# Optimization experiments

Measured on AMD Instinct MI355X. Metric: run time of the kernel, lower is better.

## Reference

```python
import jax, jax.numpy as jnp
import numpy as np
import math

EPS = 1e-9
NORM = 1.0 / math.sqrt(20.0)  # num_neighbours=20 default


def _mixing(x1, x2, B, W, b):
    # nn.Bilinear (no bias): x_bi[n,k] = sum_ij x1[n,i] B[k,i,j] x2[n,j]
    x_bi = jnp.einsum('ni,kij->nkj', x1, B)
    x_bi = jnp.einsum('nkj,nj->nk', x_bi, x2)
    x = jnp.concatenate([x1, x2, x_bi], axis=-1)
    return x @ W.T + b


def _rowstd(x):
    # torch.std default: unbiased (ddof=1)
    return jnp.std(x, axis=1, ddof=1, keepdims=True)


def setup_inputs() -> dict:
    key = jax.random.key(0)
    N, E = 100000, 2000000
    DN, DE, DA_N, DA_E = 32, 32, 3, 1
    ks = jax.random.split(key, 24)

    def nrm(k, shape, fan_in):
        return jax.random.normal(k, shape, dtype=jnp.float32) / np.sqrt(fan_in)

    inp = {
        'xn': jax.random.normal(ks[0], (N, DN), dtype=jnp.float32),
        'xn_attr': jax.random.normal(ks[1], (N, DA_N), dtype=jnp.float32),
        'xe_attr': jax.random.normal(ks[2], (E, DA_E), dtype=jnp.float32),
        'xe_src': jax.random.randint(ks[3], (E,), 0, N),
        'xe_dst': jax.random.randint(ks[4], (E,), 0, N),
        # fc1: Linear(1, xe_dim); fc2: Linear(1, xn_dim)
        'W_fc1': nrm(ks[5], (DE, 1), 1), 'b_fc1': jnp.zeros((DE,), jnp.float32),
        'W_fc2': nrm(ks[6], (DN, 1), 1), 'b_fc2': jnp.zeros((DN,), jnp.float32),
        # mix_xn: Mixing(DN, DA_N, DN)
        'B_mix_xn': nrm(ks[7], (DN, DN, DA_N), DN * DA_N),
        'W_mix_xn': nrm(ks[8], (DN, 2 * DN + DA_N), 2 * DN + DA_N),
        'b_mix_xn': jnp.zeros((DN,), jnp.float32),
        # nodes_to_edges.mix: Mixing(DN, DN, DN)
        'B_n2e': nrm(ks[9], (DN, DN, DN), DN * DN),
        'W_n2e': nrm(ks[10], (DN, 3 * DN), 3 * DN),
        'b_n2e': jnp.zeros((DN,), jnp.float32),
        # mix_xe: Mixing(DE, DA_E, DE)
        'B_mix_xe': nrm(ks[11], (DE, DE, DA_E), DE * DA_E),
        'W_mix_xe': nrm(ks[12], (DE, 2 * DE + DA_E), 2 * DE + DA_E),
        'b_mix_xe': jnp.zeros((DE,), jnp.float32),
        # edges_to_nodes.mix: Mixing(DE, DE, DE)
        'B_e2n': nrm(ks[13], (DE, DE, DE), DE * DE),
        'W_e2n': nrm(ks[14], (DE, 3 * DE), 3 * DE),
        'b_e2n': jnp.zeros((DE,), jnp.float32),
    }
    return inp


def reference(xn, xn_attr, xe_attr, xe_src, xe_dst,
              W_fc1, b_fc1, W_fc2, b_fc2,
              B_mix_xn, W_mix_xn, b_mix_xn,
              B_n2e, W_n2e, b_n2e,
              B_mix_xe, W_mix_xe, b_mix_xe,
              B_e2n, W_e2n, b_e2n):
    n_nodes = xn.shape[0]
    # node mixing + per-row std norm
    xn = _mixing(xn, xn_attr, B_mix_xn, W_mix_xn, b_mix_xn)
    xn = xn / (_rowstd(xn) + EPS)
    # fc1 weight: [E, xe_dim]
    w1 = jax.nn.silu(xe_attr @ W_fc1.T + b_fc1)
    # NodesToEdges: gather -> grad/ave -> mixing
    xg, xd = xn[xe_src], xn[xe_dst]
    xe = _mixing(w1 * (xg - xd), w1 * (xg + xd) * 0.5, B_n2e, W_n2e, b_n2e)
    xe = _mixing(xe, xe_attr, B_mix_xe, W_mix_xe, b_mix_xe)
    xe = xe / (_rowstd(xe) + EPS)
    # fc2 weight: [E, xn_dim]
    w2 = jax.nn.silu(xe_attr @ W_fc2.T + b_fc2)
    # EdgesToNodes: scatter-add over dst/src, diff/sum, mixing
    wxe = w2 * xe
    xn1 = jax.ops.segment_sum(wxe, xe_dst, num_segments=n_nodes) * NORM
    xn2 = jax.ops.segment_sum(wxe, xe_src, num_segments=n_nodes) * NORM
    xn = _mixing(xn1 - xn2, xn1 + xn2, B_e2n, W_e2n, b_e2n)
    xn = jax.nn.silu(xn)
    xn = xn / (_rowstd(xn) + EPS)
    return xn
```

## Files before the change

### kernel.cpp

```cpp
#include <hip/hip_runtime.h>
#include <hip/hip_bf16.h>

#define N_NODES 100000
#define N_EDGES 2000000
#define EPS 1e-9f
#define NORMC 0.22360679774997896f

#define BKSZ   256
#define NBK1   391
#define NBK    782
#define NSB    256
#define CE     7813
#define NITEMS 4000000

typedef short s8 __attribute__((ext_vector_type(8)));
typedef float f4 __attribute__((ext_vector_type(4)));

__device__ __forceinline__ float silu_f(float x) {
    return x / (1.0f + __expf(-x));
}

__device__ __forceinline__ ushort f2bfu(float f) {
    union { __hip_bfloat16 b; ushort u; } cv;
    cv.b = __float2bfloat16(f);
    return cv.u;
}

__device__ __forceinline__ uint pkbf(float lo, float hi) {
    float2 t; t.x = lo; t.y = hi;
    union { __hip_bfloat162 b; uint u; } cv;
    cv.b = __float22bfloat162_rn(t);
    return cv.u;
}


__device__ float mext(const float* __restrict__ W, const float* __restrict__ B,
                      const float* __restrict__ bias, int n, int i, int j) {
    if (i < 32 && j < 32) {
        float r = 0.f;
        #pragma unroll
        for (int m = 0; m < 32; ++m) r += W[n*96 + 64 + m] * B[m*1024 + i*32 + j];
        return r;
    }
    if (i < 32) return W[n*96 + i];
    if (j < 32) return W[n*96 + 32 + j];
    return bias[n];
}

__global__ void prep_kernel(const float* __restrict__ W_n2e, const float* __restrict__ B_n2e,
                            const float* __restrict__ b_n2e,
                            const float* __restrict__ W_e2n, const float* __restrict__ B_e2n,
                            const float* __restrict__ b_e2n,
                            const float* __restrict__ W_mix_xn, const float* __restrict__ B_mix_xn,
                            const float* __restrict__ b_mix_xn,
                            const float* __restrict__ W_mix_xe, const float* __restrict__ B_mix_xe,
                            const float* __restrict__ b_mix_xe,
                            ushort* __restrict__ MF, ushort* __restrict__ MG,
                            float* __restrict__ BpN, float* __restrict__ WxE,
                            float* __restrict__ CtE) {
    int t = blockIdx.x * blockDim.x + threadIdx.x;
    if (t < 69632) {
        int u = (t < 34816) ? t : t - 34816;
        int tt = u & 7, lane = (u >> 3) & 63, rest = u >> 9;
        int nt = rest & 1, kk = rest >> 1;
        int n = nt*16 + (lane & 15);
        int kl = ((lane >> 4) & 3) * 8 + tt;
        int i, j;
        if (kk < 33) { i = kk; j = kl; } else { i = kl; j = 32; }
        if (t < 34816) MF[u] = f2bfu(mext(W_n2e, B_n2e, b_n2e, n, i, j));
        else           MG[u] = f2bfu(mext(W_e2n, B_e2n, b_e2n, n, i, j));
    } else if (t < 73856) {
        int u = t - 69632;
        int k = u & 31, ij = u >> 5;
        int i = ij >> 2, j = ij & 3;
        float r;
        if (i < 32 && j < 3) {
            r = 0.f;
            #pragma unroll
            for (int m = 0; m < 32; ++m) r += W_mix_xn[k*67 + 35 + m] * B_mix_xn[m*96 + i*3 + j];
        } else if (i < 32 && j == 3) {
            r = W_mix_xn[k*67 + i];
        } else if (i == 32 && j < 3) {
            r = W_mix_xn[k*67 + 32 + j];
        } else {
            r = b_mix_xn[k];
        }
        BpN[ij*32 + k] = r;
    } else if (t < 74912) {
        int u = t - 73856;
        int k = u & 31, i = u >> 5;
        WxE[i*32 + k] = (i < 32) ? W_mix_xe[k*65 + i] : b_mix_xe[k];
    } else if (t < 75968) {
        int u = t - 74912;
        int k = u & 31, i = u >> 5;
        float r;
        if (i < 32) {
            r = 0.f;
            #pragma unroll
            for (int m = 0; m < 32; ++m) r += W_mix_xe[k*65 + 33 + m] * B_mix_xe[m*32 + i];
        } else {
            r = W_mix_xe[k*65 + 32];
        }
        CtE[i*32 + k] = r;
    }
}

__global__ void zero_kernel(float4* __restrict__ p, int n4) {
    int i = blockIdx.x * blockDim.x + threadIdx.x;
    int stride = gridDim.x * blockDim.x;
    float4 z = {0.f, 0.f, 0.f, 0.f};
    for (; i < n4; i += stride) p[i] = z;
}

__global__ __launch_bounds__(256) void node_kernel(
    const float* __restrict__ xn, const float* __restrict__ xn_attr,
    const float* __restrict__ BpN, float* __restrict__ xn_norm) {
    int n = blockIdx.x * 256 + threadIdx.x;
    if (n >= N_NODES) return;
    float x[33];
    const float4* xr = (const float4*)(xn + (size_t)n * 32);
    #pragma unroll
    for (int q = 0; q < 8; ++q) {
        float4 v = xr[q];
        x[q*4+0] = v.x; x[q*4+1] = v.y; x[q*4+2] = v.z; x[q*4+3] = v.w;
    }
    x[32] = 1.f;
    float at[4];
    at[0] = xn_attr[n*3]; at[1] = xn_attr[n*3+1]; at[2] = xn_attr[n*3+2]; at[3] = 1.f;

    float acc[32];
    #pragma unroll
    for (int k = 0; k < 32; ++k) acc[k] = 0.f;
    #pragma unroll
    for (int i = 0; i < 33; ++i) {
        #pragma unroll
        for (int j = 0; j < 4; ++j) {
            float s = x[i] * at[j];
            const float* bp = BpN + (i*4 + j) * 32;
            #pragma unroll
            for (int k = 0; k < 32; ++k) acc[k] = fmaf(bp[k], s, acc[k]);
        }
    }
    float mean = 0.f;
    #pragma unroll
    for (int k = 0; k < 32; ++k) mean += acc[k];
    mean *= (1.0f / 32.0f);
    float var = 0.f;
    #pragma unroll
    for (int k = 0; k < 32; ++k) { float d = acc[k] - mean; var += d * d; }
    var *= (1.0f / 31.0f);
    float inv = 1.0f / (sqrtf(var) + EPS);
    float4* out = (float4*)(xn_norm + (size_t)n * 32);
    #pragma unroll
    for (int q = 0; q < 8; ++q) {
        float4 v;
        v.x = acc[q*4+0]*inv; v.y = acc[q*4+1]*inv; v.z = acc[q*4+2]*inv; v.w = acc[q*4+3]*inv;
        out[q] = v;
    }
}


__global__ __launch_bounds__(256) void count_kernel(
    const int* __restrict__ xe_src, const int* __restrict__ xe_dst,
    int* __restrict__ cntg) {
    __shared__ int cnt[NBK];
    int tid = threadIdx.x, b = blockIdx.x;
    for (int k = tid; k < NBK; k += 256) cnt[k] = 0;
    __syncthreads();
    int e0 = b * CE;
    for (int i = tid; i < CE; i += 256) {
        int e = e0 + i;
        if (e < N_EDGES) {
            atomicAdd(&cnt[xe_dst[e] >> 8], 1);
            atomicAdd(&cnt[NBK1 + (xe_src[e] >> 8)], 1);
        }
    }
    __syncthreads();
    for (int k = tid; k < NBK; k += 256) cntg[k * NSB + b] = cnt[k];
}

#define SCAN_TOT (NBK * NSB)

__global__ __launch_bounds__(1024) void scan_kernel(
    const int* __restrict__ cntg, int* __restrict__ scang) {
    __shared__ int part[1024];
    int t = threadIdx.x;
    const int CHUNK = 196;
    int base = t * CHUNK;
    int s = 0;
    for (int i = 0; i < CHUNK; ++i) {
        int idx = base + i;
        if (idx < SCAN_TOT) s += cntg[idx];
    }
    part[t] = s;
    __syncthreads();
    for (int off = 1; off < 1024; off <<= 1) {
        int v = part[t];
        int add = (t >= off) ? part[t - off] : 0;
        __syncthreads();
        part[t] = v + add;
        __syncthreads();
    }
    int run = (t == 0) ? 0 : part[t - 1];
    for (int i = 0; i < CHUNK; ++i) {
        int idx = base + i;
        if (idx < SCAN_TOT) {
            int c = cntg[idx];
            scang[idx] = run;
            run += c;
        }
    }
}

__global__ __launch_bounds__(256) void scatter_kernel(
    const int* __restrict__ xe_src, const int* __restrict__ xe_dst,
    const int* __restrict__ scang, int* __restrict__ bucketed) {
    __shared__ int cur[NBK];
    int tid = threadIdx.x, b = blockIdx.x;
    for (int k = tid; k < NBK; k += 256) cur[k] = scang[k * NSB + b];
    __syncthreads();
    int e0 = b * CE;
    for (int i = tid; i < CE; i += 256) {
        int e = e0 + i;
        if (e < N_EDGES) {
            int d = xe_dst[e];
            int p = atomicAdd(&cur[d >> 8], 1);
            bucketed[p] = e | ((d & 255) << 21);
            int s_ = xe_src[e];
            p = atomicAdd(&cur[NBK1 + (s_ >> 8)], 1);
            bucketed[p] = e | ((s_ & 255) << 21);
        }
    }
}

__global__ __launch_bounds__(256) void gather_kernel(
    const ushort* __restrict__ wxe, const int* __restrict__ bucketed,
    const int* __restrict__ scang, float* __restrict__ sd0) {
    __shared__ float accs[BKSZ * 33];
    int tid = threadIdx.x, bk = blockIdx.x;
    for (int i = tid; i < BKSZ * 33; i += 256) accs[i] = 0.f;
    __syncthreads();
    int start = scang[bk * NSB];
    int end = (bk == NBK - 1) ? NITEMS : scang[(bk + 1) * NSB];
    int q = tid >> 2, g = tid & 3;
    uint4 z4; z4.x = 0u; z4.y = 0u; z4.z = 0u; z4.w = 0u;

    int i0 = start + q;
    int p0 = (i0 < end) ? bucketed[i0] : 0;
    int p1 = (i0 + 64 < end) ? bucketed[i0 + 64] : 0;
    uint4 r0 = (i0 < end)
             ? *(const uint4*)(wxe + (size_t)(p0 & 0x1FFFFF) * 32 + g * 8) : z4;

    for (int i = i0; i < end; i += 64) {
        int pn = (i + 128 < end) ? bucketed[i + 128] : 0;
        uint4 r1 = (i + 64 < end)
                 ? *(const uint4*)(wxe + (size_t)(p1 & 0x1FFFFF) * 32 + g * 8) : z4;
        int ln = (p0 >> 21) & 255;
        float* ap = &accs[ln * 33 + g * 8];
        uint uu[4] = {r0.x, r0.y, r0.z, r0.w};
        #pragma unroll
        for (int c = 0; c < 4; ++c) {
            uint u = uu[c];
            atomicAdd(&ap[c*2],     __uint_as_float((u & 0xFFFFu) << 16));
            atomicAdd(&ap[c*2 + 1], __uint_as_float(u & 0xFFFF0000u));
        }
        p0 = p1; p1 = pn; r0 = r1;
    }
    __syncthreads();
    int side = (bk < NBK1) ? 0 : 1;
    int nb = side ? bk - NBK1 : bk;
    float* out = sd0 + (size_t)side * 3211264 + (size_t)nb * BKSZ * 32;
    for (int i = tid; i < BKSZ * 32; i += 256) {
        int node = i >> 5, k = i & 31;
        out[i] = accs[node * 33 + k];
    }
}


__device__ __forceinline__ void gemm33(const ushort* __restrict__ sM,
                                       float* __restrict__ a_f,
                                       const ushort* __restrict__ ab,
                                       const float* __restrict__ biasv, int tid) {
    int lane = tid & 63, wv = tid >> 6;
    int m = lane & 15, h = lane >> 4;
    int base = wv * 64;
    float bfv[4][8];
    s8 araw[4];
    #pragma unroll
    for (int g = 0; g < 4; ++g) {
        const ushort* rp = &ab[(size_t)(base + g*16 + m) * 72];
        union { s8 v; ushort s[8]; } braw;
        braw.v = *(const s8*)&rp[h*8];
        #pragma unroll
        for (int t = 0; t < 8; ++t) {
            union { uint u; float f; } cv; cv.u = ((uint)braw.s[t]) << 16;
            bfv[g][t] = cv.f;
        }
        araw[g] = *(const s8*)&rp[32 + h*8];
    }
    f4 c[4][2];
    #pragma unroll
    for (int g = 0; g < 4; ++g) {
        c[g][0] = (f4){0.f, 0.f, 0.f, 0.f};
        c[g][1] = (f4){0.f, 0.f, 0.f, 0.f};
    }
    const s8* M8 = (const s8*)sM;
    #pragma unroll
    for (int kk = 0; kk < 33; ++kk) {
        s8 mf0 = M8[(kk*2 + 0)*64 + lane];
        s8 mf1 = M8[(kk*2 + 1)*64 + lane];
        #pragma unroll
        for (int g = 0; g < 4; ++g) {
            float as = a_f[(size_t)(base + g*16 + m) * 33 + kk];
            union { s8 v; uint u[4]; } af;
            #pragma unroll
            for (int t = 0; t < 4; ++t) af.u[t] = pkbf(as * bfv[g][2*t], as * bfv[g][2*t+1]);
            c[g][0] = __builtin_amdgcn_mfma_f32_16x16x32_bf16(af.v, mf0, c[g][0], 0, 0, 0);
            c[g][1] = __builtin_amdgcn_mfma_f32_16x16x32_bf16(af.v, mf1, c[g][1], 0, 0, 0);
        }
    }
    {
        s8 mf0 = M8[66*64 + lane];
        s8 mf1 = M8[67*64 + lane];
        #pragma unroll
        for (int g = 0; g < 4; ++g) {
            c[g][0] = __builtin_amdgcn_mfma_f32_16x16x32_bf16(araw[g], mf0, c[g][0], 0, 0, 0);
            c[g][1] = __builtin_amdgcn_mfma_f32_16x16x32_bf16(araw[g], mf1, c[g][1], 0, 0, 0);
        }
    }
    float b0 = biasv[m], b1 = biasv[16 + m];
    #pragma unroll
    for (int g = 0; g < 4; ++g) {
        int rowb = base + g*16 + h*4;
        #pragma unroll
        for (int r = 0; r < 4; ++r) {
            a_f[(size_t)(rowb + r) * 33 + m]      = c[g][0][r] + b0;
            a_f[(size_t)(rowb + r) * 33 + 16 + m] = c[g][1][r] + b1;
        }
    }
}

#define TILES_E 7813

template<bool STORE>
__global__ __launch_bounds__(256, 1) void edge_kernel(
    const float* __restrict__ xn_norm, const float* __restrict__ xe_attr,
    const int* __restrict__ xe_src, const int* __restrict__ xe_dst,
    const float* __restrict__ W_fc1, const float* __restrict__ b_fc1,
    const float* __restrict__ W_fc2, const float* __restrict__ b_fc2,
    const ushort* __restrict__ MF, const float* __restrict__ biasE,
    const float* __restrict__ WxE, const float* __restrict__ CtE,
    float* __restrict__ acc1, float* __restrict__ acc2,
    ushort* __restrict__ wxe) {
    __shared__ __align__(16) ushort sM[34816];
    __shared__ __align__(16) float  a_f[256 * 33];
    __shared__ __align__(16) ushort ab[256 * 72];
    int tid = threadIdx.x;
    {
        const float4* s4p = (const float4*)MF;
        float4* d4p = (float4*)sM;
        #pragma unroll
        for (int i = 0; i < 17; ++i) d4p[tid + i*256] = s4p[tid + i*256];
    }
    uint* ab32 = (uint*)ab;

    int t = blockIdx.x;
    float attrP = 0.f; int srcP = 0, dstP = 0; bool okP = false;
    float4 gP[8], dP[8];
    {
        int e = t*256 + tid;
        okP = e < N_EDGES;
        int ec = okP ? e : 0;
        attrP = xe_attr[ec]; srcP = xe_src[ec]; dstP = xe_dst[ec];
        const float4* gp = (const float4*)(xn_norm + (size_t)srcP * 32);
        const float4* dp = (const float4*)(xn_norm + (size_t)dstP * 32);
        #pragma unroll
        for (int q = 0; q < 8; ++q) { gP[q] = gp[q]; dP[q] = dp[q]; }
    }

    for (; t < TILES_E; t += 256) {
        float attr = attrP; int csrc = srcP, cdst = dstP; bool okC = okP;
        float vs = okC ? 1.f : 0.f;
        #pragma unroll
        for (int q = 0; q < 8; ++q) {
            float4 g = gP[q], d = dP[q];
            float gg[4] = {g.x, g.y, g.z, g.w};
            float dd[4] = {d.x, d.y, d.z, d.w};
            #pragma unroll
            for (int p = 0; p < 2; ++p) {
                int k = q*4 + p*2;
                float w0 = silu_f(attr * W_fc1[k]   + b_fc1[k])   * vs;
                float w1 = silu_f(attr * W_fc1[k+1] + b_fc1[k+1]) * vs;
                float av0 = w0 * (gg[2*p]   - dd[2*p]);
                float av1 = w1 * (gg[2*p+1] - dd[2*p+1]);
                float bv0 = w0 * (gg[2*p]   + dd[2*p])   * 0.5f;
                float bv1 = w1 * (gg[2*p+1] + dd[2*p+1]) * 0.5f;
                a_f[tid*33 + k]   = av0;
                a_f[tid*33 + k+1] = av1;
                ab32[tid*36 + (k>>1)]      = pkbf(bv0, bv1);
                ab32[tid*36 + 16 + (k>>1)] = pkbf(av0, av1);
            }
        }
        a_f[tid*33 + 32] = 1.f;

        int tn = t + 256;
        if (tn < TILES_E) {
            int e = tn*256 + tid;
            okP = e < N_EDGES;
            int ec = okP ? e : 0;
            attrP = xe_attr[ec]; srcP = xe_src[ec]; dstP = xe_dst[ec];
            const float4* gp = (const float4*)(xn_norm + (size_t)srcP * 32);
            const float4* dp = (const float4*)(xn_norm + (size_t)dstP * 32);
            #pragma unroll
            for (int q = 0; q < 8; ++q) { gP[q] = gp[q]; dP[q] = dp[q]; }
        }
        __syncthreads();

        gemm33(sM, a_f, ab, biasE, tid);
        __syncthreads();

        float2 y2[16];
        #pragma unroll
        for (int k2 = 0; k2 < 16; ++k2) y2[k2] = make_float2(0.f, 0.f);
        for (int i = 0; i < 33; ++i) {
            float xi = a_f[tid*33 + i];
            const float2* wx2 = (const float2*)(WxE + i * 32);
            const float2* ct2 = (const float2*)(CtE + i * 32);
            #pragma unroll
            for (int k2 = 0; k2 < 16; ++k2) {
                float2 w = wx2[k2], ctv = ct2[k2];
                float lx = fmaf(attr, ctv.x, w.x);
                float ly = fmaf(attr, ctv.y, w.y);
                y2[k2].x = fmaf(lx, xi, y2[k2].x);
                y2[k2].y = fmaf(ly, xi, y2[k2].y);
            }
        }
        float mean = 0.f;
        #pragma unroll
        for (int k2 = 0; k2 < 16; ++k2) mean += y2[k2].x + y2[k2].y;
        mean *= (1.0f / 32.0f);
        float var = 0.f;
        #pragma unroll
        for (int k2 = 0; k2 < 16; ++k2) {
            float dx = y2[k2].x - mean, dy = y2[k2].y - mean;
            var += dx*dx + dy*dy;
        }
        var *= (1.0f / 31.0f);
        float inv = 1.0f / (sqrtf(var) + EPS);

        if (okC) {
            if (STORE) {
                uint pkv[16];
                #pragma unroll
                for (int k2 = 0; k2 < 16; ++k2) {
                    float w20 = silu_f(attr * W_fc2[2*k2]   + b_fc2[2*k2]);
                    float w21 = silu_f(attr * W_fc2[2*k2+1] + b_fc2[2*k2+1]);
                    pkv[k2] = pkbf(w20 * y2[k2].x * inv, w21 * y2[k2].y * inv);
                }
                uint4* wp = (uint4*)(wxe + (size_t)(t*256 + tid) * 32);
                #pragma unroll
                for (int q = 0; q < 4; ++q) {
                    uint4 v; v.x = pkv[q*4]; v.y = pkv[q*4+1]; v.z = pkv[q*4+2]; v.w = pkv[q*4+3];
                    wp[q] = v;
                }
            } else {
                float* p1 = acc1 + (size_t)cdst * 32;
                float* p2 = acc2 + (size_t)csrc * 32;
                #pragma unroll
                for (int k = 0; k < 32; ++k) {
                    float yk = (k & 1) ? y2[k>>1].y : y2[k>>1].x;
                    float w2 = silu_f(attr * W_fc2[k] + b_fc2[k]);
                    float v = w2 * yk * inv;
                    unsafeAtomicAdd(p1 + k, v);
                    unsafeAtomicAdd(p2 + k, v);
                }
            }
        }
    }
}

#define TILES_F 391

__global__ __launch_bounds__(256, 1) void final_kernel(
    const float* __restrict__ acc1, const float* __restrict__ acc2,
    const ushort* __restrict__ MG, const float* __restrict__ biasG,
    float* __restrict__ out) {
    __shared__ __align__(16) ushort sM[34816];
    __shared__ __align__(16) float  a_f[256 * 33];
    __shared__ __align__(16) ushort ab[256 * 72];
    int tid = threadIdx.x;
    {
        const float4* s4p = (const float4*)MG;
        float4* d4p = (float4*)sM;
        #pragma unroll
        for (int i = 0; i < 17; ++i) d4p[tid + i*256] = s4p[tid + i*256];
    }
    uint* ab32 = (uint*)ab;

    for (int t = blockIdx.x; t < TILES_F; t += 256) {
        int n = t*256 + tid;
        bool ok = n < N_NODES;
        int nn = ok ? n : 0;
        float vs = ok ? 1.f : 0.f;
        const float4* p1 = (const float4*)(acc1 + (size_t)nn * 32);
        const float4* p2 = (const float4*)(acc2 + (size_t)nn * 32);
        #pragma unroll
        for (int q = 0; q < 8; ++q) {
            float4 u1 = p1[q], u2 = p2[q];
            float a1[4] = {u1.x, u1.y, u1.z, u1.w};
            float a2[4] = {u2.x, u2.y, u2.z, u2.w};
            #pragma unroll
            for (int p = 0; p < 2; ++p) {
                int k = q*4 + p*2;
                float dv0 = (a1[2*p]   - a2[2*p])   * NORMC * vs;
                float dv1 = (a1[2*p+1] - a2[2*p+1]) * NORMC * vs;
                float sv0 = (a1[2*p]   + a2[2*p])   * NORMC * vs;
                float sv1 = (a1[2*p+1] + a2[2*p+1]) * NORMC * vs;
                a_f[tid*33 + k]   = dv0;
                a_f[tid*33 + k+1] = dv1;
                ab32[tid*36 + (k>>1)]      = pkbf(sv0, sv1);
                ab32[tid*36 + 16 + (k>>1)] = pkbf(dv0, dv1);
            }
        }
        a_f[tid*33 + 32] = 1.f;
        __syncthreads();

        gemm33(sM, a_f, ab, biasG, tid);
        __syncthreads();

        if (ok) {
            float z[32];
            float mean = 0.f;
            #pragma unroll
            for (int k = 0; k < 32; ++k) { z[k] = silu_f(a_f[tid*33 + k]); mean += z[k]; }
            mean *= (1.0f / 32.0f);
            float var = 0.f;
            #pragma unroll
            for (int k = 0; k < 32; ++k) { float d = z[k] - mean; var += d * d; }
            var *= (1.0f / 31.0f);
            float inv = 1.0f / (sqrtf(var) + EPS);
            float4* op = (float4*)(out + (size_t)n * 32);
            #pragma unroll
            for (int q = 0; q < 8; ++q) {
                float4 v;
                v.x = z[q*4+0]*inv; v.y = z[q*4+1]*inv; v.z = z[q*4+2]*inv; v.w = z[q*4+3]*inv;
                op[q] = v;
            }
        }
    }
}

extern "C" void kernel_launch(void* const* d_in, const int* in_sizes, int n_in,
                              void* d_out, int out_size, void* d_ws, size_t ws_size,
                              hipStream_t stream) {
    const float* xn       = (const float*)d_in[0];
    const float* xn_attr  = (const float*)d_in[1];
    const float* xe_attr  = (const float*)d_in[2];
    const int*   xe_src   = (const int*)d_in[3];
    const int*   xe_dst   = (const int*)d_in[4];
    const float* W_fc1    = (const float*)d_in[5];
    const float* b_fc1    = (const float*)d_in[6];
    const float* W_fc2    = (const float*)d_in[7];
    const float* b_fc2    = (const float*)d_in[8];
    const float* B_mix_xn = (const float*)d_in[9];
    const float* W_mix_xn = (const float*)d_in[10];
    const float* b_mix_xn = (const float*)d_in[11];
    const float* B_n2e    = (const float*)d_in[12];
    const float* W_n2e    = (const float*)d_in[13];
    const float* b_n2e    = (const float*)d_in[14];
    const float* B_mix_xe = (const float*)d_in[15];
    const float* W_mix_xe = (const float*)d_in[16];
    const float* b_mix_xe = (const float*)d_in[17];
    const float* B_e2n    = (const float*)d_in[18];
    const float* W_e2n    = (const float*)d_in[19];
    const float* b_e2n    = (const float*)d_in[20];

    float* ws = (float*)d_ws;
    const size_t MAIN_BYTES = 46065088ULL * 4ULL;
    bool big = ws_size >= MAIN_BYTES;

    if (big) {
        float*  xn_norm = ws;
        float*  sd0     = ws + 3200000;
        float*  sd1     = ws + 6411264;
        ushort* MF      = (ushort*)(ws + 9622528);
        ushort* MG      = MF + 34816;
        float*  BpN     = ws + 9657344;
        float*  WxE     = ws + 9661568;
        float*  CtE     = ws + 9662624;
        ushort* wxe     = (ushort*)(ws + 9663680);
        int*    bucketed= (int*)(ws + 41663680);
        int*    cntg    = (int*)(ws + 45663680);
        int*    scang   = (int*)(ws + 45864384);

        prep_kernel<<<297, 256, 0, stream>>>(W_n2e, B_n2e, b_n2e, W_e2n, B_e2n, b_e2n,
                                             W_mix_xn, B_mix_xn, b_mix_xn,
                                             W_mix_xe, B_mix_xe, b_mix_xe,
                                             MF, MG, BpN, WxE, CtE);
        node_kernel<<<391, 256, 0, stream>>>(xn, xn_attr, BpN, xn_norm);
        count_kernel<<<NSB, 256, 0, stream>>>(xe_src, xe_dst, cntg);
        scan_kernel<<<1, 1024, 0, stream>>>(cntg, scang);
        scatter_kernel<<<NSB, 256, 0, stream>>>(xe_src, xe_dst, scang, bucketed);
        edge_kernel<true><<<256, 256, 0, stream>>>(xn_norm, xe_attr, xe_src, xe_dst,
                                                   W_fc1, b_fc1, W_fc2, b_fc2,
                                                   MF, b_n2e, WxE, CtE,
                                                   nullptr, nullptr, wxe);
        gather_kernel<<<NBK, 256, 0, stream>>>(wxe, bucketed, scang, sd0);
        final_kernel<<<391, 256, 0, stream>>>(sd0, sd1, MG, b_e2n, (float*)d_out);
    } else {
        float*  xn_norm = ws;
        float*  acc1    = ws + 3200000;
        float*  acc2    = ws + 6400000;
        ushort* MF      = (ushort*)(ws + 9600000);
        ushort* MG      = MF + 34816;
        float*  BpN     = ws + 9600000 + 34816;
        float*  WxE     = BpN + 4224;
        float*  CtE     = WxE + 1056;

        prep_kernel<<<297, 256, 0, stream>>>(W_n2e, B_n2e, b_n2e, W_e2n, B_e2n, b_e2n,
                                             W_mix_xn, B_mix_xn, b_mix_xn,
                                             W_mix_xe, B_mix_xe, b_mix_xe,
                                             MF, MG, BpN, WxE, CtE);
        zero_kernel<<<2048, 256, 0, stream>>>((float4*)acc1, 1600000);
        node_kernel<<<391, 256, 0, stream>>>(xn, xn_attr, BpN, xn_norm);
        edge_kernel<false><<<256, 256, 0, stream>>>(xn_norm, xe_attr, xe_src, xe_dst,
                                                    W_fc1, b_fc1, W_fc2, b_fc2,
                                                    MF, b_n2e, WxE, CtE,
                                                    acc1, acc2, nullptr);
        final_kernel<<<391, 256, 0, stream>>>(acc1, acc2, MG, b_e2n, (float*)d_out);
    }
}
```

Before: 2.013 ms.

## Scatter edge outputs directly into bucketed order so gather streams sequentially

The scatter pass now records each edge's bucket positions for dst and src. The edge kernel then writes each bf16 edge result twice, straight into those bucketed slots, instead of once in edge order. The gather kernel can then read the values contiguously rather than through random indirection. The cost is a doubled write volume, extra position arrays and a larger workspace, plus random 64-byte writes in place of random reads. The count/scatter block count is also doubled and the scan is simplified with an exact chunk size.

After: 1.813 ms. 1.11x faster.

```diff
diff --git a/kernel.cpp b/kernel.cpp
--- a/kernel.cpp
+++ b/kernel.cpp
@@ -9,9 +9,11 @@
 #define BKSZ   256
 #define NBK1   391
 #define NBK    782
-#define NSB    256
-#define CE     7813
+#define NSB    512
+#define CE     3907
 #define NITEMS 4000000
+#define SCAN_TOT (NBK * NSB)
+#define SCHUNK 391
 
 typedef short s8 __attribute__((ext_vector_type(8)));
 typedef float f4 __attribute__((ext_vector_type(4)));
@@ -179,19 +181,13 @@
     for (int k = tid; k < NBK; k += 256) cntg[k * NSB + b] = cnt[k];
 }
 
-#define SCAN_TOT (NBK * NSB)
-
 __global__ __launch_bounds__(1024) void scan_kernel(
     const int* __restrict__ cntg, int* __restrict__ scang) {
     __shared__ int part[1024];
     int t = threadIdx.x;
-    const int CHUNK = 196;
-    int base = t * CHUNK;
+    int base = t * SCHUNK;
     int s = 0;
-    for (int i = 0; i < CHUNK; ++i) {
-        int idx = base + i;
-        if (idx < SCAN_TOT) s += cntg[idx];
-    }
+    for (int i = 0; i < SCHUNK; ++i) s += cntg[base + i];
     part[t] = s;
     __syncthreads();
     for (int off = 1; off < 1024; off <<= 1) {
@@ -202,19 +198,18 @@
         __syncthreads();
     }
     int run = (t == 0) ? 0 : part[t - 1];
-    for (int i = 0; i < CHUNK; ++i) {
-        int idx = base + i;
-        if (idx < SCAN_TOT) {
-            int c = cntg[idx];
-            scang[idx] = run;
-            run += c;
-        }
-    }
-}
-
+    for (int i = 0; i < SCHUNK; ++i) {
+        int c = cntg[base + i];
+        scang[base + i] = run;
+        run += c;
+    }
+}
+
+template<bool WRITE_POS>
 __global__ __launch_bounds__(256) void scatter_kernel(
     const int* __restrict__ xe_src, const int* __restrict__ xe_dst,
-    const int* __restrict__ scang, int* __restrict__ bucketed) {
+    const int* __restrict__ scang, int* __restrict__ bucketed,
+    int* __restrict__ posd, int* __restrict__ poss) {
     __shared__ int cur[NBK];
     int tid = threadIdx.x, b = blockIdx.x;
     for (int k = tid; k < NBK; k += 256) cur[k] = scang[k * NSB + b];
@@ -226,14 +221,61 @@
             int d = xe_dst[e];
             int p = atomicAdd(&cur[d >> 8], 1);
             bucketed[p] = e | ((d & 255) << 21);
+            if (WRITE_POS) posd[e] = p;
             int s_ = xe_src[e];
-            p = atomicAdd(&cur[NBK1 + (s_ >> 8)], 1);
-            bucketed[p] = e | ((s_ & 255) << 21);
-        }
-    }
-}
-
-__global__ __launch_bounds__(256) void gather_kernel(
+            int p2 = atomicAdd(&cur[NBK1 + (s_ >> 8)], 1);
+            bucketed[p2] = e | ((s_ & 255) << 21);
+            if (WRITE_POS) poss[e] = p2;
+        }
+    }
+}
+
+__global__ __launch_bounds__(256) void gather_stream(
+    const ushort* __restrict__ wxe2, const int* __restrict__ bucketed,
+    const int* __restrict__ scang, float* __restrict__ sd0) {
+    __shared__ float accs[BKSZ * 33];
+    int tid = threadIdx.x, bk = blockIdx.x;
+    for (int i = tid; i < BKSZ * 33; i += 256) accs[i] = 0.f;
+    __syncthreads();
+    int start = scang[bk * NSB];
+    int end = (bk == NBK - 1) ? NITEMS : scang[(bk + 1) * NSB];
+    int q = tid >> 2, g = tid & 3;
+    uint4 z4; z4.x = 0u; z4.y = 0u; z4.z = 0u; z4.w = 0u;
+
+    int i = start + q;
+    int ln0 = 0; uint4 r0 = z4;
+    if (i < end) {
+        ln0 = (bucketed[i] >> 21) & 255;
+        r0 = *(const uint4*)(wxe2 + (size_t)i * 32 + g * 8);
+    }
+    for (; i < end; i += 64) {
+        int in = i + 64;
+        int ln1 = 0; uint4 r1 = z4;
+        if (in < end) {
+            ln1 = (bucketed[in] >> 21) & 255;
+            r1 = *(const uint4*)(wxe2 + (size_t)in * 32 + g * 8);
+        }
+        float* ap = &accs[ln0 * 33 + g * 8];
+        uint uu[4] = {r0.x, r0.y, r0.z, r0.w};
+        #pragma unroll
+        for (int c = 0; c < 4; ++c) {
+            uint u = uu[c];
+            atomicAdd(&ap[c*2],     __uint_as_float((u & 0xFFFFu) << 16));
+            atomicAdd(&ap[c*2 + 1], __uint_as_float(u & 0xFFFF0000u));
+        }
+        ln0 = ln1; r0 = r1;
+    }
+    __syncthreads();
+    int side = (bk < NBK1) ? 0 : 1;
+    int nb = side ? bk - NBK1 : bk;
+    float* out = sd0 + (size_t)side * 3211264 + (size_t)nb * BKSZ * 32;
+    for (int i2 = tid; i2 < BKSZ * 32; i2 += 256) {
+        int node = i2 >> 5, k = i2 & 31;
+        out[i2] = accs[node * 33 + k];
+    }
+}
+
+__global__ __launch_bounds__(256) void gather_rand(
     const ushort* __restrict__ wxe, const int* __restrict__ bucketed,
     const int* __restrict__ scang, float* __restrict__ sd0) {
     __shared__ float accs[BKSZ * 33];
@@ -270,9 +312,9 @@
     int side = (bk < NBK1) ? 0 : 1;
     int nb = side ? bk - NBK1 : bk;
     float* out = sd0 + (size_t)side * 3211264 + (size_t)nb * BKSZ * 32;
-    for (int i = tid; i < BKSZ * 32; i += 256) {
-        int node = i >> 5, k = i & 31;
-        out[i] = accs[node * 33 + k];
+    for (int i2 = tid; i2 < BKSZ * 32; i2 += 256) {
+        int node = i2 >> 5, k = i2 & 31;
+        out[i2] = accs[node * 33 + k];
     }
 }
 
@@ -342,7 +384,7 @@
 
 #define TILES_E 7813
 
-template<bool STORE>
+template<int MODE>
 __global__ __launch_bounds__(256, 1) void edge_kernel(
     const float* __restrict__ xn_norm, const float* __restrict__ xe_attr,
     const int* __restrict__ xe_src, const int* __restrict__ xe_dst,
@@ -351,7 +393,8 @@
     const ushort* __restrict__ MF, const float* __restrict__ biasE,
     const float* __restrict__ WxE, const float* __restrict__ CtE,
     float* __restrict__ acc1, float* __restrict__ acc2,
-    ushort* __restrict__ wxe) {
+    ushort* __restrict__ wxe,
+    const int* __restrict__ posd, const int* __restrict__ poss) {
     __shared__ __align__(16) ushort sM[34816];
     __shared__ __align__(16) float  a_f[256 * 33];
     __shared__ __align__(16) ushort ab[256 * 72];
@@ -365,13 +408,14 @@
     uint* ab32 = (uint*)ab;
 
     int t = blockIdx.x;
-    float attrP = 0.f; int srcP = 0, dstP = 0; bool okP = false;
+    float attrP = 0.f; int srcP = 0, dstP = 0, pdP = 0, psP = 0; bool okP = false;
     float4 gP[8], dP[8];
     {
         int e = t*256 + tid;
         okP = e < N_EDGES;
         int ec = okP ? e : 0;
         attrP = xe_attr[ec]; srcP = xe_src[ec]; dstP = xe_dst[ec];
+        if (MODE == 2) { pdP = posd[ec]; psP = poss[ec]; }
         const float4* gp = (const float4*)(xn_norm + (size_t)srcP * 32);
         const float4* dp = (const float4*)(xn_norm + (size_t)dstP * 32);
         #pragma unroll
@@ -379,7 +423,8 @@
     }
 
     for (; t < TILES_E; t += 256) {
-        float attr = attrP; int csrc = srcP, cdst = dstP; bool okC = okP;
+        float attr = attrP; int csrc = srcP, cdst = dstP, cpd = pdP, cps = psP;
+        bool okC = okP;
         float vs = okC ? 1.f : 0.f;
         #pragma unroll
         for (int q = 0; q < 8; ++q) {
@@ -409,6 +454,7 @@
             okP = e < N_EDGES;
             int ec = okP ? e : 0;
             attrP = xe_attr[ec]; srcP = xe_src[ec]; dstP = xe_dst[ec];
+            if (MODE == 2) { pdP = posd[ec]; psP = poss[ec]; }
             const float4* gp = (const float4*)(xn_norm + (size_t)srcP * 32);
             const float4* dp = (const float4*)(xn_norm + (size_t)dstP * 32);
             #pragma unroll
@@ -449,7 +495,7 @@
         float inv = 1.0f / (sqrtf(var) + EPS);
 
         if (okC) {
-            if (STORE) {
+            if (MODE >= 1) {
                 uint pkv[16];
                 #pragma unroll
                 for (int k2 = 0; k2 < 16; ++k2) {
@@ -457,11 +503,21 @@
                     float w21 = silu_f(attr * W_fc2[2*k2+1] + b_fc2[2*k2+1]);
                     pkv[k2] = pkbf(w20 * y2[k2].x * inv, w21 * y2[k2].y * inv);
                 }
-                uint4* wp = (uint4*)(wxe + (size_t)(t*256 + tid) * 32);
+                uint4 v[4];
                 #pragma unroll
                 for (int q = 0; q < 4; ++q) {
-                    uint4 v; v.x = pkv[q*4]; v.y = pkv[q*4+1]; v.z = pkv[q*4+2]; v.w = pkv[q*4+3];
-                    wp[q] = v;
+                    v[q].x = pkv[q*4]; v[q].y = pkv[q*4+1];
+                    v[q].z = pkv[q*4+2]; v[q].w = pkv[q*4+3];
+                }
+                if (MODE == 1) {
+                    uint4* wp = (uint4*)(wxe + (size_t)(t*256 + tid) * 32);
+                    #pragma unroll
+                    for (int q = 0; q < 4; ++q) wp[q] = v[q];
+                } else {
+                    uint4* w1p = (uint4*)(wxe + (size_t)cpd * 32);
+                    uint4* w2p = (uint4*)(wxe + (size_t)cps * 32);
+                    #pragma unroll
+                    for (int q = 0; q < 4; ++q) { w1p[q] = v[q]; w2p[q] = v[q]; }
                 }
             } else {
                 float* p1 = acc1 + (size_t)cdst * 32;
@@ -470,9 +526,9 @@
                 for (int k = 0; k < 32; ++k) {
                     float yk = (k & 1) ? y2[k>>1].y : y2[k>>1].x;
                     float w2 = silu_f(attr * W_fc2[k] + b_fc2[k]);
-                    float v = w2 * yk * inv;
-                    unsafeAtomicAdd(p1 + k, v);
-                    unsafeAtomicAdd(p2 + k, v);
+                    float vv = w2 * yk * inv;
+                    unsafeAtomicAdd(p1 + k, vv);
+                    unsafeAtomicAdd(p2 + k, vv);
                 }
             }
         }
@@ -576,10 +632,41 @@
     const float* b_e2n    = (const float*)d_in[20];
 
     float* ws = (float*)d_ws;
-    const size_t MAIN_BYTES = 46065088ULL * 4ULL;
-    bool big = ws_size >= MAIN_BYTES;
-
-    if (big) {
+    const size_t T2_BYTES = 82464448ULL * 4ULL;
+    const size_t T1_BYTES = 46464448ULL * 4ULL;
+
+    if (ws_size >= T2_BYTES) {
+        float*  xn_norm = ws;
+        float*  sd0     = ws + 3200000;
+        float*  sd1     = ws + 6411264;
+        ushort* MF      = (ushort*)(ws + 9622528);
+        ushort* MG      = MF + 34816;
+        float*  BpN     = ws + 9657344;
+        float*  WxE     = ws + 9661568;
+        float*  CtE     = ws + 9662624;
+        ushort* wxe2    = (ushort*)(ws + 9663680);
+        int*    bucketed= (int*)(ws + 73663680);
+        int*    posd    = (int*)(ws + 77663680);
+        int*    poss    = (int*)(ws + 79663680);
+        int*    cntg    = (int*)(ws + 81663680);
+        int*    scang   = (int*)(ws + 82064064);
+
+        prep_kernel<<<297, 256, 0, stream>>>(W_n2e, B_n2e, b_n2e, W_e2n, B_e2n, b_e2n,
+                                             W_mix_xn, B_mix_xn, b_mix_xn,
+                                             W_mix_xe, B_mix_xe, b_mix_xe,
+                                             MF, MG, BpN, WxE, CtE);
+        node_kernel<<<391, 256, 0, stream>>>(xn, xn_attr, BpN, xn_norm);
+        count_kernel<<<NSB, 256, 0, stream>>>(xe_src, xe_dst, cntg);
+        scan_kernel<<<1, 1024, 0, stream>>>(cntg, scang);
+        scatter_kernel<true><<<NSB, 256, 0, stream>>>(xe_src, xe_dst, scang,
+                                                      bucketed, posd, poss);
+        edge_kernel<2><<<256, 256, 0, stream>>>(xn_norm, xe_attr, xe_src, xe_dst,
+                                                W_fc1, b_fc1, W_fc2, b_fc2,
+                                                MF, b_n2e, WxE, CtE,
+                                                nullptr, nullptr, wxe2, posd, poss);
+        gather_stream<<<NBK, 256, 0, stream>>>(wxe2, bucketed, scang, sd0);
+        final_kernel<<<391, 256, 0, stream>>>(sd0, sd1, MG, b_e2n, (float*)d_out);
+    } else if (ws_size >= T1_BYTES) {
         float*  xn_norm = ws;
         float*  sd0     = ws + 3200000;
         float*  sd1     = ws + 6411264;
@@ -591,7 +678,7 @@
         ushort* wxe     = (ushort*)(ws + 9663680);
         int*    bucketed= (int*)(ws + 41663680);
         int*    cntg    = (int*)(ws + 45663680);
-        int*    scang   = (int*)(ws + 45864384);
+        int*    scang   = (int*)(ws + 46064064);
 
         prep_kernel<<<297, 256, 0, stream>>>(W_n2e, B_n2e, b_n2e, W_e2n, B_e2n, b_e2n,
                                              W_mix_xn, B_mix_xn, b_mix_xn,
@@ -600,12 +687,13 @@
         node_kernel<<<391, 256, 0, stream>>>(xn, xn_attr, BpN, xn_norm);
         count_kernel<<<NSB, 256, 0, stream>>>(xe_src, xe_dst, cntg);
         scan_kernel<<<1, 1024, 0, stream>>>(cntg, scang);
-        scatter_kernel<<<NSB, 256, 0, stream>>>(xe_src, xe_dst, scang, bucketed);
-        edge_kernel<true><<<256, 256, 0, stream>>>(xn_norm, xe_attr, xe_src, xe_dst,
-                                                   W_fc1, b_fc1, W_fc2, b_fc2,
-                                                   MF, b_n2e, WxE, CtE,
-                                                   nullptr, nullptr, wxe);
-        gather_kernel<<<NBK, 256, 0, stream>>>(wxe, bucketed, scang, sd0);
+        scatter_kernel<false><<<NSB, 256, 0, stream>>>(xe_src, xe_dst, scang,
+                                                       bucketed, nullptr, nullptr);
+        edge_kernel<1><<<256, 256, 0, stream>>>(xn_norm, xe_attr, xe_src, xe_dst,
+                                                W_fc1, b_fc1, W_fc2, b_fc2,
+                                                MF, b_n2e, WxE, CtE,
+                                                nullptr, nullptr, wxe, nullptr, nullptr);
+        gather_rand<<<NBK, 256, 0, stream>>>(wxe, bucketed, scang, sd0);
         final_kernel<<<391, 256, 0, stream>>>(sd0, sd1, MG, b_e2n, (float*)d_out);
     } else {
         float*  xn_norm = ws;
@@ -623,10 +711,10 @@
                                              MF, MG, BpN, WxE, CtE);
         zero_kernel<<<2048, 256, 0, stream>>>((float4*)acc1, 1600000);
         node_kernel<<<391, 256, 0, stream>>>(xn, xn_attr, BpN, xn_norm);
-        edge_kernel<false><<<256, 256, 0, stream>>>(xn_norm, xe_attr, xe_src, xe_dst,
-                                                    W_fc1, b_fc1, W_fc2, b_fc2,
-                                                    MF, b_n2e, WxE, CtE,
-                                                    acc1, acc2, nullptr);
+        edge_kernel<0><<<256, 256, 0, stream>>>(xn_norm, xe_attr, xe_src, xe_dst,
+                                                W_fc1, b_fc1, W_fc2, b_fc2,
+                                                MF, b_n2e, WxE, CtE,
+                                                acc1, acc2, nullptr, nullptr, nullptr);
         final_kernel<<<391, 256, 0, stream>>>(acc1, acc2, MG, b_e2n, (float*)d_out);
     }
 }
```

## Batch gather through LDS staging and double count/scatter block count

Applied to the files above, without the earlier changes.

The gather kernel now has each thread load one full 64-byte bf16 edge row (four uint4) and stage it in shared memory. Threads then cooperatively atomic-add staged rows into the per-bucket accumulators, prefetching the next chunk while the current one is processed. The count/scatter kernels use 512 blocks of about 3907 edges instead of 256, and the scan and workspace layout are resized to match. This aims for more memory-level parallelism in the gather and better occupancy in bucketing, at the cost of extra LDS traffic, syncs and a larger single-block scan.

Result: faster. 1.848 ms (-8.2%).

```diff
diff --git a/kernel.cpp b/kernel.cpp
--- a/kernel.cpp
+++ b/kernel.cpp
@@ -9,9 +9,12 @@
 #define BKSZ   256
 #define NBK1   391
 #define NBK    782
-#define NSB    256
-#define CE     7813
+#define NSB    512
+#define CE     3907
 #define NITEMS 4000000
+#define SCAN_TOT (NBK * NSB)
+#define SCHUNK 391
+#define GCHUNK 256
 
 typedef short s8 __attribute__((ext_vector_type(8)));
 typedef float f4 __attribute__((ext_vector_type(4)));
@@ -179,19 +182,13 @@
     for (int k = tid; k < NBK; k += 256) cntg[k * NSB + b] = cnt[k];
 }
 
-#define SCAN_TOT (NBK * NSB)
-
 __global__ __launch_bounds__(1024) void scan_kernel(
     const int* __restrict__ cntg, int* __restrict__ scang) {
     __shared__ int part[1024];
     int t = threadIdx.x;
-    const int CHUNK = 196;
-    int base = t * CHUNK;
+    int base = t * SCHUNK;
     int s = 0;
-    for (int i = 0; i < CHUNK; ++i) {
-        int idx = base + i;
-        if (idx < SCAN_TOT) s += cntg[idx];
-    }
+    for (int i = 0; i < SCHUNK; ++i) s += cntg[base + i];
     part[t] = s;
     __syncthreads();
     for (int off = 1; off < 1024; off <<= 1) {
@@ -202,13 +199,10 @@
         __syncthreads();
     }
     int run = (t == 0) ? 0 : part[t - 1];
-    for (int i = 0; i < CHUNK; ++i) {
-        int idx = base + i;
-        if (idx < SCAN_TOT) {
-            int c = cntg[idx];
-            scang[idx] = run;
-            run += c;
-        }
+    for (int i = 0; i < SCHUNK; ++i) {
+        int c = cntg[base + i];
+        scang[base + i] = run;
+        run += c;
     }
 }
 
@@ -227,52 +221,75 @@
             int p = atomicAdd(&cur[d >> 8], 1);
             bucketed[p] = e | ((d & 255) << 21);
             int s_ = xe_src[e];
-            p = atomicAdd(&cur[NBK1 + (s_ >> 8)], 1);
-            bucketed[p] = e | ((s_ & 255) << 21);
-        }
-    }
-}
-
-__global__ __launch_bounds__(256) void gather_kernel(
+            int p2 = atomicAdd(&cur[NBK1 + (s_ >> 8)], 1);
+            bucketed[p2] = e | ((s_ & 255) << 21);
+        }
+    }
+}
+
+__global__ __launch_bounds__(256) void gather_batch(
     const ushort* __restrict__ wxe, const int* __restrict__ bucketed,
     const int* __restrict__ scang, float* __restrict__ sd0) {
     __shared__ float accs[BKSZ * 33];
+    __shared__ uint  stage[GCHUNK * 17];
     int tid = threadIdx.x, bk = blockIdx.x;
     for (int i = tid; i < BKSZ * 33; i += 256) accs[i] = 0.f;
-    __syncthreads();
     int start = scang[bk * NSB];
     int end = (bk == NBK - 1) ? NITEMS : scang[(bk + 1) * NSB];
-    int q = tid >> 2, g = tid & 3;
-    uint4 z4; z4.x = 0u; z4.y = 0u; z4.z = 0u; z4.w = 0u;
-
-    int i0 = start + q;
-    int p0 = (i0 < end) ? bucketed[i0] : 0;
-    int p1 = (i0 + 64 < end) ? bucketed[i0 + 64] : 0;
-    uint4 r0 = (i0 < end)
-             ? *(const uint4*)(wxe + (size_t)(p0 & 0x1FFFFF) * 32 + g * 8) : z4;
-
-    for (int i = i0; i < end; i += 64) {
-        int pn = (i + 128 < end) ? bucketed[i + 128] : 0;
-        uint4 r1 = (i + 64 < end)
-                 ? *(const uint4*)(wxe + (size_t)(p1 & 0x1FFFFF) * 32 + g * 8) : z4;
-        int ln = (p0 >> 21) & 255;
-        float* ap = &accs[ln * 33 + g * 8];
-        uint uu[4] = {r0.x, r0.y, r0.z, r0.w};
-        #pragma unroll
-        for (int c = 0; c < 4; ++c) {
-            uint u = uu[c];
-            atomicAdd(&ap[c*2],     __uint_as_float((u & 0xFFFFu) << 16));
-            atomicAdd(&ap[c*2 + 1], __uint_as_float(u & 0xFFFF0000u));
-        }
-        p0 = p1; p1 = pn; r0 = r1;
+    int last = (end > start) ? (end - 1) : 0;
+
+    uint4 r0, r1, r2, r3; int ln = 0; uint msk = 0;
+    {
+        int idx = start + tid;
+        msk = (idx < end) ? 0xFFFFFFFFu : 0u;
+        int cl = (idx < end) ? idx : last;
+        int p = bucketed[cl];
+        ln = (p >> 21) & 255;
+        const uint4* wp = (const uint4*)(wxe + (size_t)(p & 0x1FFFFF) * 32);
+        r0 = wp[0]; r1 = wp[1]; r2 = wp[2]; r3 = wp[3];
     }
     __syncthreads();
+
+    for (int base = start; base < end; base += GCHUNK) {
+        uint* sp = &stage[tid * 17];
+        sp[0]=r0.x&msk;  sp[1]=r0.y&msk;  sp[2]=r0.z&msk;  sp[3]=r0.w&msk;
+        sp[4]=r1.x&msk;  sp[5]=r1.y&msk;  sp[6]=r1.z&msk;  sp[7]=r1.w&msk;
+        sp[8]=r2.x&msk;  sp[9]=r2.y&msk;  sp[10]=r2.z&msk; sp[11]=r2.w&msk;
+        sp[12]=r3.x&msk; sp[13]=r3.y&msk; sp[14]=r3.z&msk; sp[15]=r3.w&msk;
+        sp[16] = (uint)ln;
+        __syncthreads();
+        int nbase = base + GCHUNK;
+        if (nbase < end) {
+            int idx = nbase + tid;
+            msk = (idx < end) ? 0xFFFFFFFFu : 0u;
+            int cl = (idx < end) ? idx : last;
+            int p = bucketed[cl];
+            ln = (p >> 21) & 255;
+            const uint4* wp = (const uint4*)(wxe + (size_t)(p & 0x1FFFFF) * 32);
+            r0 = wp[0]; r1 = wp[1]; r2 = wp[2]; r3 = wp[3];
+        }
+        int jq = tid >> 2, g = tid & 3;
+        #pragma unroll
+        for (int rr = 0; rr < 4; ++rr) {
+            const uint* q = &stage[(jq + 64*rr) * 17];
+            int lnj = (int)q[16];
+            float* ap = &accs[lnj * 33 + g * 8];
+            #pragma unroll
+            for (int c = 0; c < 4; ++c) {
+                uint u = q[g * 4 + c];
+                atomicAdd(&ap[c*2],     __uint_as_float((u & 0xFFFFu) << 16));
+                atomicAdd(&ap[c*2 + 1], __uint_as_float(u & 0xFFFF0000u));
+            }
+        }
+        __syncthreads();
+    }
+
     int side = (bk < NBK1) ? 0 : 1;
     int nb = side ? bk - NBK1 : bk;
     float* out = sd0 + (size_t)side * 3211264 + (size_t)nb * BKSZ * 32;
-    for (int i = tid; i < BKSZ * 32; i += 256) {
-        int node = i >> 5, k = i & 31;
-        out[i] = accs[node * 33 + k];
+    for (int i2 = tid; i2 < BKSZ * 32; i2 += 256) {
+        int node = i2 >> 5, k = i2 & 31;
+        out[i2] = accs[node * 33 + k];
     }
 }
 
@@ -342,7 +359,7 @@
 
 #define TILES_E 7813
 
-template<bool STORE>
+template<int MODE>
 __global__ __launch_bounds__(256, 1) void edge_kernel(
     const float* __restrict__ xn_norm, const float* __restrict__ xe_attr,
     const int* __restrict__ xe_src, const int* __restrict__ xe_dst,
@@ -379,7 +396,8 @@
     }
 
     for (; t < TILES_E; t += 256) {
-        float attr = attrP; int csrc = srcP, cdst = dstP; bool okC = okP;
+        float attr = attrP; int csrc = srcP, cdst = dstP;
+        bool okC = okP;
         float vs = okC ? 1.f : 0.f;
         #pragma unroll
         for (int q = 0; q < 8; ++q) {
@@ -449,7 +467,7 @@
         float inv = 1.0f / (sqrtf(var) + EPS);
 
         if (okC) {
-            if (STORE) {
+            if (MODE == 1) {
                 uint pkv[16];
                 #pragma unroll
                 for (int k2 = 0; k2 < 16; ++k2) {
@@ -470,9 +488,9 @@
                 for (int k = 0; k < 32; ++k) {
                     float yk = (k & 1) ? y2[k>>1].y : y2[k>>1].x;
                     float w2 = silu_f(attr * W_fc2[k] + b_fc2[k]);
-                    float v = w2 * yk * inv;
-                    unsafeAtomicAdd(p1 + k, v);
-                    unsafeAtomicAdd(p2 + k, v);
+                    float vv = w2 * yk * inv;
+                    unsafeAtomicAdd(p1 + k, vv);
+                    unsafeAtomicAdd(p2 + k, vv);
                 }
             }
         }
@@ -576,10 +594,9 @@
     const float* b_e2n    = (const float*)d_in[20];
 
     float* ws = (float*)d_ws;
-    const size_t MAIN_BYTES = 46065088ULL * 4ULL;
-    bool big = ws_size >= MAIN_BYTES;
-
-    if (big) {
+    const size_t T1_BYTES = 46464448ULL * 4ULL;
+
+    if (ws_size >= T1_BYTES) {
         float*  xn_norm = ws;
         float*  sd0     = ws + 3200000;
         float*  sd1     = ws + 6411264;
@@ -591,7 +608,7 @@
         ushort* wxe     = (ushort*)(ws + 9663680);
         int*    bucketed= (int*)(ws + 41663680);
         int*    cntg    = (int*)(ws + 45663680);
-        int*    scang   = (int*)(ws + 45864384);
+        int*    scang   = (int*)(ws + 46064064);
 
         prep_kernel<<<297, 256, 0, stream>>>(W_n2e, B_n2e, b_n2e, W_e2n, B_e2n, b_e2n,
                                              W_mix_xn, B_mix_xn, b_mix_xn,
@@ -601,11 +618,11 @@
         count_kernel<<<NSB, 256, 0, stream>>>(xe_src, xe_dst, cntg);
         scan_kernel<<<1, 1024, 0, stream>>>(cntg, scang);
         scatter_kernel<<<NSB, 256, 0, stream>>>(xe_src, xe_dst, scang, bucketed);
-        edge_kernel<true><<<256, 256, 0, stream>>>(xn_norm, xe_attr, xe_src, xe_dst,
-                                                   W_fc1, b_fc1, W_fc2, b_fc2,
-                                                   MF, b_n2e, WxE, CtE,
-                                                   nullptr, nullptr, wxe);
-        gather_kernel<<<NBK, 256, 0, stream>>>(wxe, bucketed, scang, sd0);
+        edge_kernel<1><<<256, 256, 0, stream>>>(xn_norm, xe_attr, xe_src, xe_dst,
+                                                W_fc1, b_fc1, W_fc2, b_fc2,
+                                                MF, b_n2e, WxE, CtE,
+                                                nullptr, nullptr, wxe);
+        gather_batch<<<NBK, 256, 0, stream>>>(wxe, bucketed, scang, sd0);
         final_kernel<<<391, 256, 0, stream>>>(sd0, sd1, MG, b_e2n, (float*)d_out);
     } else {
         float*  xn_norm = ws;
@@ -623,10 +640,10 @@
                                              MF, MG, BpN, WxE, CtE);
         zero_kernel<<<2048, 256, 0, stream>>>((float4*)acc1, 1600000);
         node_kernel<<<391, 256, 0, stream>>>(xn, xn_attr, BpN, xn_norm);
-        edge_kernel<false><<<256, 256, 0, stream>>>(xn_norm, xe_attr, xe_src, xe_dst,
-                                                    W_fc1, b_fc1, W_fc2, b_fc2,
-                                                    MF, b_n2e, WxE, CtE,
-                                                    acc1, acc2, nullptr);
+        edge_kernel<0><<<256, 256, 0, stream>>>(xn_norm, xe_attr, xe_src, xe_dst,
+                                                W_fc1, b_fc1, W_fc2, b_fc2,
+                                                MF, b_n2e, WxE, CtE,
+                                                acc1, acc2, nullptr);
         final_kernel<<<391, 256, 0, stream>>>(acc1, acc2, MG, b_e2n, (float*)d_out);
     }
 }
```
